# Kernel tuning notes

Hardware: AMD Instinct MI355X
Metric: run time of the kernel (lower is better)

Reference implementation:

```python
import jax, jax.numpy as jnp
import numpy as np

B, S = 256, 512          # batch, seqlen
M = 128                  # memory_size
DK = 128                 # memory_key_state_dim == q_embed_dim == final_fc_dim
DV = 256                 # memory_value_state_dim == qa_embed_dim
NQ = 10000               # n_question
FC = 128                 # final_fc_dim


def _kaiming(key, shape):
    fan_in = shape[-1]
    return jax.random.normal(key, shape, dtype=jnp.float32) * np.float32(np.sqrt(2.0 / fan_in))


def setup_inputs() -> dict:
    key = jax.random.key(0)
    ks = jax.random.split(key, 12)
    q_data = jax.random.randint(ks[0], (B, S), 0, NQ + 1)
    qa_data = jax.random.randint(ks[1], (B, S), 0, 2 * NQ + 1)
    # embedding tables (padding_idx=0 -> zero row)
    q_embed_table = _kaiming(ks[2], (NQ + 1, DK)).at[0].set(0.0)
    qa_embed_table = _kaiming(ks[3], (2 * NQ + 1, DV)).at[0].set(0.0)
    memory_key = _kaiming(ks[4], (M, DK))
    init_memory_value = _kaiming(ks[5], (M, DV))
    W_erase = _kaiming(ks[6], (DV, DV)); b_erase = jnp.zeros((DV,), jnp.float32)
    W_add = _kaiming(ks[7], (DV, DV)); b_add = jnp.zeros((DV,), jnp.float32)
    W_read = _kaiming(ks[8], (FC, DV + FC)); b_read = jnp.zeros((FC,), jnp.float32)
    W_pred = _kaiming(ks[9], (1, FC)); b_pred = jnp.zeros((1,), jnp.float32)
    return {
        "q_data": q_data, "qa_data": qa_data,
        "q_embed_table": q_embed_table, "qa_embed_table": qa_embed_table,
        "memory_key": memory_key, "init_memory_value": init_memory_value,
        "W_erase": W_erase, "b_erase": b_erase,
        "W_add": W_add, "b_add": b_add,
        "W_read": W_read, "b_read": b_read,
        "W_pred": W_pred, "b_pred": b_pred,
    }


def reference(q_data, qa_data, q_embed_table, qa_embed_table, memory_key,
              init_memory_value, W_erase, b_erase, W_add, b_add,
              W_read, b_read, W_pred, b_pred):
    batch = q_data.shape[0]
    qe = q_embed_table[q_data]      # [B,S,DK]
    qae = qa_embed_table[qa_data]   # [B,S,DV]

    def step(mem, inp):
        q_t, qa_t = inp  # [B,DK], [B,DV]
        # key addressing: tiny matmul + softmax
        w = jax.nn.softmax(q_t @ memory_key.T, axis=1)            # [B,M]
        # weighted read from value memory
        read = jnp.einsum('bm,bmd->bd', w, mem)                   # [B,DV]
        # gated erase/add write
        e = jax.nn.sigmoid(qa_t @ W_erase.T + b_erase)            # [B,DV]
        a = jnp.tanh(qa_t @ W_add.T + b_add)                      # [B,DV]
        mem = mem * (1.0 - w[:, :, None] * e[:, None, :]) + w[:, :, None] * a[:, None, :]
        return mem, read

    mem0 = jnp.broadcast_to(init_memory_value, (batch,) + init_memory_value.shape)
    _, reads = jax.lax.scan(step, mem0, (qe.transpose(1, 0, 2), qae.transpose(1, 0, 2)))
    reads = reads.transpose(1, 0, 2)                              # [B,S,DV]

    predict_input = jnp.concatenate([reads, qe], axis=-1)         # [B,S,DV+FC]
    h = jnp.tanh(predict_input @ W_read.T + b_read)               # [B,S,FC]
    logits = h @ W_pred.T + b_pred                                # [B,S,1]
    return logits[..., 0]
```

## Files before the change

kernel.cpp:

```cpp
#include <hip/hip_runtime.h>
#include <hip/hip_bf16.h>


#define BB    256
#define SS    512
#define MM    128
#define DKk   128
#define DVv   256

typedef float  f32x2  __attribute__((ext_vector_type(2)));
typedef float  f32x4  __attribute__((ext_vector_type(4)));
typedef short  bf16x8 __attribute__((ext_vector_type(8)));

static __device__ __forceinline__ unsigned short f2bf(float f) {
    unsigned u = __float_as_uint(f);
    unsigned r = (u + 0x7FFFu + ((u >> 16) & 1u)) >> 16;
    return (unsigned short)r;
}
static __device__ __forceinline__ float bf2f(unsigned short u) {
    return __uint_as_float(((unsigned)u) << 16);
}
static __device__ __forceinline__ float fast_tanh(float x) {
    float ex = __expf(2.f * x);
    return 1.f - 2.f / (ex + 1.f);
}
static __device__ __forceinline__ float fast_sigmoid(float x) {
    return 1.f / (1.f + __expf(-x));
}

__global__ __launch_bounds__(256) void kcvt(const float* __restrict__ qa_tab,
                                            const float* __restrict__ q_tab,
                                            const float* __restrict__ W_er,
                                            const float* __restrict__ W_ad,
                                            const float* __restrict__ W_rd,
                                            const float* __restrict__ mk,
                                            unsigned short* __restrict__ qa16,
                                            unsigned short* __restrict__ q16,
                                            unsigned short* __restrict__ wea16,
                                            unsigned short* __restrict__ wrd16,
                                            unsigned short* __restrict__ mk16,
                                            int n_qa, int n_q) {
    for (int i = blockIdx.x * 256 + threadIdx.x; i < n_qa; i += gridDim.x * 256)
        qa16[i] = f2bf(qa_tab[i]);
    for (int i = blockIdx.x * 256 + threadIdx.x; i < n_q; i += gridDim.x * 256)
        q16[i] = f2bf(q_tab[i]);
    for (int i = blockIdx.x * 256 + threadIdx.x; i < 65536; i += gridDim.x * 256) {
        wea16[i] = f2bf(W_er[i]);
        wea16[65536 + i] = f2bf(W_ad[i]);
    }
    for (int i = blockIdx.x * 256 + threadIdx.x; i < 49152; i += gridDim.x * 256)
        wrd16[i] = f2bf(W_rd[i]);
    for (int i = blockIdx.x * 256 + threadIdx.x; i < 16384; i += gridDim.x * 256)
        mk16[i] = f2bf(mk[i]);
}

__global__ __launch_bounds__(256) void k1_mfma(const int* __restrict__ q_data,
                                               const unsigned short* __restrict__ q16,
                                               const unsigned short* __restrict__ mk16,
                                               float* __restrict__ w_buf,
                                               int tcs, int tcm, int coff) {
    __shared__ __align__(16) unsigned short A_lds[128 * 64];
    __shared__ int qidx[128];
    int t = threadIdx.x;
    int row0 = blockIdx.x * 128;
    if (t < 128) {
        int rl = row0 + t;
        qidx[t] = q_data[(rl >> tcs) * SS + coff + (rl & tcm)];
    }
    int l = t & 63;
    int wid = t >> 6;
    f32x4 acc[2][8];
    #pragma unroll
    for (int i = 0; i < 2; ++i)
        #pragma unroll
        for (int j = 0; j < 8; ++j)
            acc[i][j] = (f32x4){0.f, 0.f, 0.f, 0.f};

    for (int ks = 0; ks < 128; ks += 64) {
        __syncthreads();
        #pragma unroll
        for (int p = 0; p < 4; ++p) {
            int U = p * 256 + t;
            int r = U >> 3, kb = U & 7;
            int kb_log = kb ^ (r & 7);
            int4 v = *reinterpret_cast<const int4*>(q16 + (size_t)qidx[r] * DKk + ks + kb_log * 8);
            *reinterpret_cast<int4*>(&A_lds[U * 8]) = v;
        }
        __syncthreads();
        #pragma unroll
        for (int ksub = 0; ksub < 2; ++ksub) {
            bf16x8 af[2];
            #pragma unroll
            for (int mi = 0; mi < 2; ++mi) {
                int r = wid * 32 + mi * 16 + (l & 15);
                int kb_log = ksub * 4 + (l >> 4);
                int pu = r * 8 + (kb_log ^ (r & 7));
                af[mi] = *reinterpret_cast<const bf16x8*>(&A_lds[pu * 8]);
            }
            #pragma unroll
            for (int nj = 0; nj < 8; ++nj) {
                int col = nj * 16 + (l & 15);
                bf16x8 bf = *reinterpret_cast<const bf16x8*>(
                    mk16 + (size_t)col * DKk + ks + ksub * 32 + (l >> 4) * 8);
                #pragma unroll
                for (int mi = 0; mi < 2; ++mi)
                    acc[mi][nj] = __builtin_amdgcn_mfma_f32_16x16x32_bf16(af[mi], bf, acc[mi][nj], 0, 0, 0);
            }
        }
    }
    #pragma unroll
    for (int mi = 0; mi < 2; ++mi) {
        #pragma unroll
        for (int reg = 0; reg < 4; ++reg) {
            float mx = acc[mi][0][reg];
            #pragma unroll
            for (int nj = 1; nj < 8; ++nj) mx = fmaxf(mx, acc[mi][nj][reg]);
            #pragma unroll
            for (int off = 1; off < 16; off <<= 1) mx = fmaxf(mx, __shfl_xor(mx, off, 64));
            float p[8], s = 0.f;
            #pragma unroll
            for (int nj = 0; nj < 8; ++nj) { p[nj] = __expf(acc[mi][nj][reg] - mx); s += p[nj]; }
            #pragma unroll
            for (int off = 1; off < 16; off <<= 1) s += __shfl_xor(s, off, 64);
            float inv = 1.f / s;
            int row = row0 + wid * 32 + mi * 16 + (l >> 4) * 4 + reg;
            #pragma unroll
            for (int nj = 0; nj < 8; ++nj)
                w_buf[(size_t)row * MM + nj * 16 + (l & 15)] = p[nj] * inv;
        }
    }
}

__global__ __launch_bounds__(256) void k2_ea_mfma(const int* __restrict__ qa_data,
                                                  const unsigned short* __restrict__ qa16,
                                                  const unsigned short* __restrict__ wea16,
                                                  const float* __restrict__ b_er,
                                                  const float* __restrict__ b_ad,
                                                  unsigned short* __restrict__ ea16,
                                                  int tcs, int tcm, int coff) {
    __shared__ __align__(16) unsigned short A_lds[128 * 64];
    __shared__ int qidx[128];
    int t = threadIdx.x;
    int rb = blockIdx.x >> 2, cb = blockIdx.x & 3;
    int row0 = rb * 128;
    if (t < 128) {
        int rl = row0 + t;
        qidx[t] = qa_data[(rl >> tcs) * SS + coff + (rl & tcm)];
    }
    int l = t & 63;
    int wid = t >> 6, wr = wid >> 1, wc = wid & 1;
    f32x4 acc[4][4];
    #pragma unroll
    for (int i = 0; i < 4; ++i)
        #pragma unroll
        for (int j = 0; j < 4; ++j)
            acc[i][j] = (f32x4){0.f, 0.f, 0.f, 0.f};

    for (int ks = 0; ks < 256; ks += 64) {
        __syncthreads();
        #pragma unroll
        for (int p = 0; p < 4; ++p) {
            int U = p * 256 + t;
            int r = U >> 3, kb = U & 7;
            int kb_log = kb ^ (r & 7);
            int4 v = *reinterpret_cast<const int4*>(qa16 + (size_t)qidx[r] * 256 + ks + kb_log * 8);
            *reinterpret_cast<int4*>(&A_lds[U * 8]) = v;
        }
        __syncthreads();
        #pragma unroll
        for (int ksub = 0; ksub < 2; ++ksub) {
            bf16x8 af[4];
            #pragma unroll
            for (int mi = 0; mi < 4; ++mi) {
                int r = wr * 64 + mi * 16 + (l & 15);
                int kb_log = ksub * 4 + (l >> 4);
                int pu = r * 8 + (kb_log ^ (r & 7));
                af[mi] = *reinterpret_cast<const bf16x8*>(&A_lds[pu * 8]);
            }
            #pragma unroll
            for (int nj = 0; nj < 4; ++nj) {
                int col = cb * 128 + wc * 64 + nj * 16 + (l & 15);
                bf16x8 bf = *reinterpret_cast<const bf16x8*>(
                    wea16 + (size_t)col * 256 + ks + ksub * 32 + (l >> 4) * 8);
                #pragma unroll
                for (int mi = 0; mi < 4; ++mi)
                    acc[mi][nj] = __builtin_amdgcn_mfma_f32_16x16x32_bf16(af[mi], bf, acc[mi][nj], 0, 0, 0);
            }
        }
    }
    #pragma unroll
    for (int nj = 0; nj < 4; ++nj) {
        int col = cb * 128 + wc * 64 + nj * 16 + (l & 15);
        bool is_e = (cb < 2);
        float bias = is_e ? b_er[col] : b_ad[col - 256];
        #pragma unroll
        for (int mi = 0; mi < 4; ++mi) {
            #pragma unroll
            for (int reg = 0; reg < 4; ++reg) {
                int rl = row0 + wr * 64 + mi * 16 + (l >> 4) * 4 + reg;
                float x = acc[mi][nj][reg] + bias;
                float y = is_e ? fast_sigmoid(x) : fast_tanh(x);
                ea16[(size_t)rl * 512 + col] = f2bf(y);
            }
        }
    }
}

__global__ __launch_bounds__(1024, 1) void k3_seq(const float* __restrict__ w_buf,
                                                  const unsigned short* __restrict__ ea16,
                                                  const float* __restrict__ init_mem,
                                                  float* __restrict__ state,
                                                  unsigned short* __restrict__ reads16,
                                                  int TC, int first, int last) {
    __shared__ float rdlds[8][4][256];
    int b = blockIdx.x;
    int tid = threadIdx.x;
    int wv = tid >> 6, lane = tid & 63;
    int mq = wv >> 2, dq = wv & 3;
    int d = dq * 64 + lane;
    int m0 = mq * 32;
    f32x2 mem[16];
    if (first) {
        #pragma unroll
        for (int i = 0; i < 16; ++i) {
            mem[i].x = init_mem[(size_t)(m0 + 2 * i) * DVv + d];
            mem[i].y = init_mem[(size_t)(m0 + 2 * i + 1) * DVv + d];
        }
    } else {
        #pragma unroll
        for (int i = 0; i < 16; ++i)
            mem[i] = *reinterpret_cast<const f32x2*>(&state[((size_t)b * DVv + d) * MM + m0 + 2 * i]);
    }
    size_t rb = (size_t)b * TC;
    for (int t0 = 0; t0 < TC; t0 += 8) {
        f32x4 w4 = *reinterpret_cast<const f32x4*>(
            w_buf + (rb + t0 + (lane >> 3)) * MM + m0 + (lane & 7) * 4);
        float e8[8], a8[8];
        #pragma unroll
        for (int g = 0; g < 8; ++g) {
            const unsigned short* ep = ea16 + (rb + t0 + g) * 512;
            e8[g] = bf2f(ep[d]);
            a8[g] = bf2f(ep[256 + d]);
        }
        #pragma unroll
        for (int g = 0; g < 8; ++g) {
            f32x2 rd; rd.x = 0.f; rd.y = 0.f;
            f32x2 ne2; ne2.x = -e8[g]; ne2.y = -e8[g];
            f32x2 a2;  a2.x = a8[g];  a2.y = a8[g];
            #pragma unroll
            for (int i = 0; i < 16; ++i) {
                int src = 8 * g + (i >> 1);
                int c = (i & 1) * 2;
                f32x2 ws;
                ws.x = __uint_as_float((unsigned)__builtin_amdgcn_readlane(__float_as_uint(w4[c]), src));
                ws.y = __uint_as_float((unsigned)__builtin_amdgcn_readlane(__float_as_uint(w4[c + 1]), src));
                f32x2 tt;
                asm("v_pk_fma_f32 %0, %1, %2, %0" : "+v"(rd)     : "s"(ws), "v"(mem[i]));
                asm("v_pk_fma_f32 %0, %1, %2, %3" : "=v"(tt)     : "v"(ne2), "v"(mem[i]), "v"(a2));
                asm("v_pk_fma_f32 %0, %1, %2, %0" : "+v"(mem[i]) : "s"(ws), "v"(tt));
            }
            rdlds[g][mq][d] = rd.x + rd.y;
        }
        __syncthreads();
        #pragma unroll
        for (int r = 0; r < 2; ++r) {
            int idx = tid + r * 1024;
            int g = idx >> 8, dd = idx & 255;
            float s = rdlds[g][0][dd] + rdlds[g][1][dd] + rdlds[g][2][dd] + rdlds[g][3][dd];
            reads16[(rb + t0 + g) * DVv + dd] = f2bf(s);
        }
        __syncthreads();
    }
    if (!last) {
        #pragma unroll
        for (int i = 0; i < 16; ++i)
            *reinterpret_cast<f32x2*>(&state[((size_t)b * DVv + d) * MM + m0 + 2 * i]) = mem[i];
    }
}

__global__ __launch_bounds__(256) void k4_mfma(const int* __restrict__ q_data,
                                               const unsigned short* __restrict__ q16,
                                               const unsigned short* __restrict__ reads16,
                                               const unsigned short* __restrict__ wrd16,
                                               const float* __restrict__ b_rd,
                                               const float* __restrict__ W_pr,
                                               const float* __restrict__ b_pr,
                                               float* __restrict__ out,
                                               int tcs, int tcm, int coff) {
    __shared__ __align__(16) unsigned short A_lds[128 * 64];
    __shared__ int qidx[128];
    __shared__ float plds[2][128];
    int t = threadIdx.x;
    int row0 = blockIdx.x * 128;
    if (t < 128) {
        int rl = row0 + t;
        qidx[t] = q_data[(rl >> tcs) * SS + coff + (rl & tcm)];
    }
    int l = t & 63;
    int wid = t >> 6, wr = wid >> 1, wc = wid & 1;
    f32x4 acc[4][4];
    #pragma unroll
    for (int i = 0; i < 4; ++i)
        #pragma unroll
        for (int j = 0; j < 4; ++j)
            acc[i][j] = (f32x4){0.f, 0.f, 0.f, 0.f};

    for (int ks = 0; ks < 384; ks += 64) {
        __syncthreads();
        #pragma unroll
        for (int p = 0; p < 4; ++p) {
            int U = p * 256 + t;
            int r = U >> 3, kb = U & 7;
            int kb_log = kb ^ (r & 7);
            int kg = ks + kb_log * 8;
            const unsigned short* src = (kg < 256)
                ? (reads16 + (size_t)(row0 + r) * DVv + kg)
                : (q16 + (size_t)qidx[r] * DKk + (kg - 256));
            int4 v = *reinterpret_cast<const int4*>(src);
            *reinterpret_cast<int4*>(&A_lds[U * 8]) = v;
        }
        __syncthreads();
        #pragma unroll
        for (int ksub = 0; ksub < 2; ++ksub) {
            bf16x8 af[4];
            #pragma unroll
            for (int mi = 0; mi < 4; ++mi) {
                int r = wr * 64 + mi * 16 + (l & 15);
                int kb_log = ksub * 4 + (l >> 4);
                int pu = r * 8 + (kb_log ^ (r & 7));
                af[mi] = *reinterpret_cast<const bf16x8*>(&A_lds[pu * 8]);
            }
            #pragma unroll
            for (int nj = 0; nj < 4; ++nj) {
                int col = wc * 64 + nj * 16 + (l & 15);
                bf16x8 bf = *reinterpret_cast<const bf16x8*>(
                    wrd16 + (size_t)col * 384 + ks + ksub * 32 + (l >> 4) * 8);
                #pragma unroll
                for (int mi = 0; mi < 4; ++mi)
                    acc[mi][nj] = __builtin_amdgcn_mfma_f32_16x16x32_bf16(af[mi], bf, acc[mi][nj], 0, 0, 0);
            }
        }
    }
    float part[16];
    #pragma unroll
    for (int k = 0; k < 16; ++k) part[k] = 0.f;
    #pragma unroll
    for (int nj = 0; nj < 4; ++nj) {
        int col = wc * 64 + nj * 16 + (l & 15);
        float bias = b_rd[col];
        float wpr = W_pr[col];
        #pragma unroll
        for (int mi = 0; mi < 4; ++mi) {
            #pragma unroll
            for (int reg = 0; reg < 4; ++reg) {
                float h = fast_tanh(acc[mi][nj][reg] + bias);
                part[mi * 4 + reg] = fmaf(h, wpr, part[mi * 4 + reg]);
            }
        }
    }
    #pragma unroll
    for (int k = 0; k < 16; ++k) {
        #pragma unroll
        for (int off = 1; off < 16; off <<= 1)
            part[k] += __shfl_xor(part[k], off, 64);
    }
    if ((l & 15) == 0) {
        #pragma unroll
        for (int mi = 0; mi < 4; ++mi)
            #pragma unroll
            for (int reg = 0; reg < 4; ++reg) {
                int row = wr * 64 + mi * 16 + (l >> 4) * 4 + reg;
                plds[wc][row] = part[mi * 4 + reg];
            }
    }
    __syncthreads();
    if (t < 128) {
        float s = plds[0][t] + plds[1][t] + b_pr[0];
        int rl = row0 + t;
        out[(rl >> tcs) * SS + coff + (rl & tcm)] = s;
    }
}

extern "C" void kernel_launch(void* const* d_in, const int* in_sizes, int n_in,
                              void* d_out, int out_size, void* d_ws, size_t ws_size,
                              hipStream_t stream) {
    const int*   q_data   = (const int*)d_in[0];
    const int*   qa_data  = (const int*)d_in[1];
    const float* q_tab    = (const float*)d_in[2];
    const float* qa_tab   = (const float*)d_in[3];
    const float* mk       = (const float*)d_in[4];
    const float* init_mem = (const float*)d_in[5];
    const float* W_er     = (const float*)d_in[6];
    const float* b_er     = (const float*)d_in[7];
    const float* W_ad     = (const float*)d_in[8];
    const float* b_ad     = (const float*)d_in[9];
    const float* W_rd     = (const float*)d_in[10];
    const float* b_rd     = (const float*)d_in[11];
    const float* W_pr     = (const float*)d_in[12];
    const float* b_pr     = (const float*)d_in[13];
    float* out = (float*)d_out;

    const size_t state_f = (size_t)BB * MM * DVv;
    const size_t qa16_n  = (size_t)in_sizes[3];
    const size_t q16_n   = (size_t)in_sizes[2];
    const size_t wea16_n = 131072;
    const size_t wrd16_n = 49152;
    const size_t mk16_n  = 16384;
    const size_t bf16_f  = (qa16_n + q16_n + wea16_n + wrd16_n + mk16_n) / 2 + 32;

    size_t avail_f = ws_size / 4;
    int TC = 8;
    {
        const int cand[] = {512, 256, 128, 64, 32, 16, 8};
        for (int i = 0; i < 7; ++i) {
            size_t need = state_f + bf16_f + (size_t)BB * cand[i] * (MM + 256 + 128);
            if (need <= avail_f) { TC = cand[i]; break; }
        }
    }
    int NC = SS / TC;
    int tcs = __builtin_ctz(TC);
    int tcm = TC - 1;

    float* ws      = (float*)d_ws;
    float* state   = ws;
    float* w_buf   = state + state_f;
    unsigned short* ea16    = (unsigned short*)(w_buf + (size_t)BB * TC * MM);
    unsigned short* reads16 = ea16 + (size_t)BB * TC * 512;
    unsigned short* qa16  = reads16 + (size_t)BB * TC * DVv;
    unsigned short* q16   = qa16 + qa16_n;
    unsigned short* wea16 = q16 + q16_n;
    unsigned short* wrd16 = wea16 + wea16_n;
    unsigned short* mk16  = wrd16 + wrd16_n;

    kcvt<<<1024, 256, 0, stream>>>(qa_tab, q_tab, W_er, W_ad, W_rd, mk,
                                   qa16, q16, wea16, wrd16, mk16,
                                   (int)qa16_n, (int)q16_n);
    for (int c = 0; c < NC; ++c) {
        int coff = c * TC;
        int rows = BB * TC;
        k1_mfma<<<rows / 128, 256, 0, stream>>>(q_data, q16, mk16, w_buf, tcs, tcm, coff);
        k2_ea_mfma<<<(rows / 128) * 4, 256, 0, stream>>>(qa_data, qa16, wea16, b_er, b_ad,
                                                         ea16, tcs, tcm, coff);
        k3_seq<<<BB, 1024, 0, stream>>>(w_buf, ea16, init_mem, state, reads16,
                                        TC, c == 0, c == NC - 1);
        k4_mfma<<<rows / 128, 256, 0, stream>>>(q_data, q16, reads16, wrd16, b_rd, W_pr, b_pr,
                                                out, tcs, tcm, coff);
    }
}
```

Baseline: 609.9 us.

## Load attention weights as wave-uniform scalars with double-buffered prefetch in scan kernel

```diff
diff --git a/kernel.cpp b/kernel.cpp
--- a/kernel.cpp
+++ b/kernel.cpp
@@ -232,9 +232,17 @@
             mem[i] = *reinterpret_cast<const f32x2*>(&state[((size_t)b * DVv + d) * MM + m0 + 2 * i]);
     }
     size_t rb = (size_t)b * TC;
+    unsigned wrow = (unsigned)__builtin_amdgcn_readfirstlane((int)((unsigned)rb * MM + m0));
+    const f32x2* wbase2 = reinterpret_cast<const f32x2*>(w_buf + wrow);
+    int tcl = TC - 1;
+
+    f32x2 wA[16], wB[16];
+    #pragma unroll
+    for (int j = 0; j < 16; ++j) wA[j] = wbase2[j];
+    #pragma unroll
+    for (int j = 0; j < 16; ++j) wB[j] = wbase2[16 + j];
+
     for (int t0 = 0; t0 < TC; t0 += 8) {
-        f32x4 w4 = *reinterpret_cast<const f32x4*>(
-            w_buf + (rb + t0 + (lane >> 3)) * MM + m0 + (lane & 7) * 4);
         float e8[8], a8[8];
         #pragma unroll
         for (int g = 0; g < 8; ++g) {
@@ -242,25 +250,26 @@
             e8[g] = bf2f(ep[d]);
             a8[g] = bf2f(ep[256 + d]);
         }
-        #pragma unroll
-        for (int g = 0; g < 8; ++g) {
-            f32x2 rd; rd.x = 0.f; rd.y = 0.f;
-            f32x2 ne2; ne2.x = -e8[g]; ne2.y = -e8[g];
-            f32x2 a2;  a2.x = a8[g];  a2.y = a8[g];
-            #pragma unroll
-            for (int i = 0; i < 16; ++i) {
-                int src = 8 * g + (i >> 1);
-                int c = (i & 1) * 2;
-                f32x2 ws;
-                ws.x = __uint_as_float((unsigned)__builtin_amdgcn_readlane(__float_as_uint(w4[c]), src));
-                ws.y = __uint_as_float((unsigned)__builtin_amdgcn_readlane(__float_as_uint(w4[c + 1]), src));
-                f32x2 tt;
-                asm("v_pk_fma_f32 %0, %1, %2, %0" : "+v"(rd)     : "s"(ws), "v"(mem[i]));
-                asm("v_pk_fma_f32 %0, %1, %2, %3" : "=v"(tt)     : "v"(ne2), "v"(mem[i]), "v"(a2));
-                asm("v_pk_fma_f32 %0, %1, %2, %0" : "+v"(mem[i]) : "s"(ws), "v"(tt));
-            }
-            rdlds[g][mq][d] = rd.x + rd.y;
-        }
+        #define K3_STEP(G, WCUR)                                                              \
+        {                                                                                     \
+            f32x2 rd; rd.x = 0.f; rd.y = 0.f;                                                 \
+            f32x2 ne2; ne2.x = -e8[G]; ne2.y = -e8[G];                                        \
+            f32x2 a2;  a2.x = a8[G];  a2.y = a8[G];                                           \
+            _Pragma("unroll")                                                                 \
+            for (int i = 0; i < 16; ++i) {                                                    \
+                f32x2 tt;                                                                     \
+                asm("v_pk_fma_f32 %0, %1, %2, %0" : "+v"(rd)     : "s"(WCUR[i]), "v"(mem[i]));\
+                asm("v_pk_fma_f32 %0, %1, %2, %3" : "=v"(tt)     : "v"(ne2), "v"(mem[i]), "v"(a2)); \
+                asm("v_pk_fma_f32 %0, %1, %2, %0" : "+v"(mem[i]) : "s"(WCUR[i]), "v"(tt));    \
+            }                                                                                 \
+            rdlds[G][mq][d] = rd.x + rd.y;                                                    \
+            int tp = t0 + G + 2; tp = (tp < tcl) ? tp : tcl;                                  \
+            _Pragma("unroll")                                                                 \
+            for (int j = 0; j < 16; ++j) WCUR[j] = wbase2[tp * 16 + j];                       \
+        }
+        K3_STEP(0, wA) K3_STEP(1, wB) K3_STEP(2, wA) K3_STEP(3, wB)
+        K3_STEP(4, wA) K3_STEP(5, wB) K3_STEP(6, wA) K3_STEP(7, wB)
+        #undef K3_STEP
         __syncthreads();
         #pragma unroll
         for (int r = 0; r < 2; ++r) {
@@ -411,8 +420,8 @@
     size_t avail_f = ws_size / 4;
     int TC = 8;
     {
-        const int cand[] = {512, 256, 128, 64, 32, 16, 8};
-        for (int i = 0; i < 7; ++i) {
+        const int cand[] = {128, 64, 32, 16, 8};
+        for (int i = 0; i < 5; ++i) {
             size_t need = state_f + bf16_f + (size_t)BB * cand[i] * (MM + 256 + 128);
             if (need <= avail_f) { TC = cand[i]; break; }
         }
@@ -438,9 +447,9 @@
     for (int c = 0; c < NC; ++c) {
         int coff = c * TC;
         int rows = BB * TC;
-        k1_mfma<<<rows / 128, 256, 0, stream>>>(q_data, q16, mk16, w_buf, tcs, tcm, coff);
         k2_ea_mfma<<<(rows / 128) * 4, 256, 0, stream>>>(qa_data, qa16, wea16, b_er, b_ad,
                                                          ea16, tcs, tcm, coff);
+        k1_mfma<<<rows / 128, 256, 0, stream>>>(q_data, q16, mk16, w_buf, tcs, tcm, coff);
         k3_seq<<<BB, 1024, 0, stream>>>(w_buf, ea16, init_mem, state, reads16,
                                         TC, c == 0, c == NC - 1);
         k4_mfma<<<rows / 128, 256, 0, stream>>>(q_data, q16, reads16, wrd16, b_rd, W_pr, b_pr,
```

New measurement: 648.3 us. +6.3%, slower.
